# Optimization experiments

Measured on AMD Instinct MI355X. Metric: run time of the kernel, lower is better.

Reference implementation:

```python
import jax, jax.numpy as jnp
import numpy as np

B, N, C, H = 64, 197, 768, 12
CH = C // H            # 64 head dim
RC = CH // 2           # 32 reduced channel
RN = N // 8            # 24 reduced tokens
TOPK_COEF = 8
BUDGET = int(np.ceil(0.25 * N))   # 50
BASIS_THRESH = 0.02
MP_SCALE = H ** -0.5               # MaskPredictor: num_heads**-0.5 (as in source)
ATTN_SCALE = CH ** -0.5
LN_EPS = 1e-5


def _ln(x, g, b):
    mu = x.mean(-1, keepdims=True)
    var = ((x - mu) ** 2).mean(-1, keepdims=True)
    return (x - mu) * jax.lax.rsqrt(var + LN_EPS) * g + b


def _keep_topk(x, k):
    # zero all but the k largest along last axis (tie-break by value threshold)
    kth = jax.lax.top_k(x, k)[0][..., -1:]
    return jnp.where(x >= kth, x, 0.0)


def setup_inputs() -> dict:
    key = jax.random.key(0)
    ks = jax.random.split(key, 20)
    d = {}
    d['x'] = jax.random.normal(ks[0], (B, N, C), jnp.float32)
    s = 0.02
    d['Wqkv'] = jax.random.normal(ks[1], (C, 3 * C), jnp.float32) * s
    d['Wcq'] = jax.random.normal(ks[2], (CH, RC), jnp.float32) * s
    d['bcq'] = jnp.zeros((RC,), jnp.float32)
    d['Wck'] = jax.random.normal(ks[3], (CH, RC), jnp.float32) * s
    d['bck'] = jnp.zeros((RC,), jnp.float32)
    d['proj_n'] = jax.random.normal(ks[4], (N, RN), jnp.float32) * s
    d['proj_back_n'] = jax.random.normal(ks[5], (N, RN), jnp.float32) * s
    d['Wproj'] = jax.random.normal(ks[6], (C, C), jnp.float32) * s
    d['bproj'] = jnp.zeros((C,), jnp.float32)
    d['g1'] = jnp.ones((C,), jnp.float32)
    d['b1'] = jnp.zeros((C,), jnp.float32)
    d['g2'] = jnp.ones((C,), jnp.float32)
    d['b2'] = jnp.zeros((C,), jnp.float32)
    d['W1'] = jax.random.normal(ks[7], (C, 4 * C), jnp.float32) * s
    d['bfc1'] = jnp.zeros((4 * C,), jnp.float32)
    d['W2'] = jax.random.normal(ks[8], (4 * C, C), jnp.float32) * s
    d['bfc2'] = jnp.zeros((C,), jnp.float32)
    return d


def reference(x, Wqkv, Wcq, bcq, Wck, bck, proj_n, proj_back_n, Wproj, bproj,
              g1, b1, g2, b2, W1, bfc1, W2, bfc2):
    h = _ln(x, g1, b1)
    qkv = (h @ Wqkv).reshape(B, N, 3, H, CH).transpose(2, 0, 3, 1, 4)  # [3,B,H,N,CH]
    q, k, v = qkv[0], qkv[1], qkv[2]

    # ---- MaskPredictor (eval path) ----
    qp = q @ Wcq + bcq                                # [B,H,N,RC]
    kp = k @ Wck + bck                                # [B,H,N,RC]
    kk = jnp.einsum('bhnc,nr->bhcr', kp, proj_n)      # [B,H,RC,RN]
    cheap = jnp.einsum('bhnc,bhcr->bhnr', qp, kk) * MP_SCALE
    cheap = cheap[:, :, 1:, :]                        # drop cls query row
    basis_coef = jax.nn.softmax(cheap, axis=-1)       # [B,H,N-1,RN]
    basis_coef = _keep_topk(basis_coef, TOPK_COEF)
    basis = jnp.abs(proj_back_n.T)                    # [RN,N]
    basis = jnp.where(basis > BASIS_THRESH, basis, 0.0)
    approx_attn = basis_coef @ basis                  # [B,H,N-1,N]
    kth = jax.lax.top_k(approx_attn, BUDGET)[0][..., -1:]
    mask = approx_attn >= kth                         # [B,H,N-1,N] bool
    cls_mask = jnp.ones((B, H, 1, N), bool)
    attn_mask = jnp.concatenate([cls_mask, mask], axis=2)  # [B,H,N,N]

    # ---- masked full attention ----
    attn = jnp.einsum('bhqc,bhkc->bhqk', q * ATTN_SCALE, k)
    attn = jnp.where(attn_mask, attn, -jnp.inf)
    attn = jax.nn.softmax(attn, axis=-1)
    out = jnp.einsum('bhqk,bhkc->bhqc', attn, v)
    out = out.transpose(0, 2, 1, 3).reshape(B, N, C)
    out = out @ Wproj + bproj

    x = x + out                                       # skip_lam = 1.0
    h2 = _ln(x, g2, b2)
    mlp = jax.nn.gelu(h2 @ W1 + bfc1, approximate=False) @ W2 + bfc2
    x = x + mlp
    return x
```

## Files before the change

### kernel.cpp

```cpp
#include <hip/hip_runtime.h>
#include <math.h>
#include <float.h>

#define B_ 64
#define N_ 197
#define C_ 768
#define H_ 12
#define CH_ 64
#define RC_ 32
#define RN_ 24

typedef __attribute__((ext_vector_type(8))) short short8;
typedef __attribute__((ext_vector_type(4))) float f32x4;
typedef __attribute__((address_space(3))) void  lds_void;
typedef __attribute__((address_space(1))) const void g_void;

__device__ __forceinline__ float warp_sum(float v){
  #pragma unroll
  for(int o=32;o>=1;o>>=1) v += __shfl_xor(v,o);
  return v;
}
__device__ __forceinline__ float warp_max(float v){
  #pragma unroll
  for(int o=32;o>=1;o>>=1) v = fmaxf(v,__shfl_xor(v,o));
  return v;
}
__device__ __forceinline__ unsigned short f2bf(float f){
  union{float f; unsigned u;} c; c.f = f;
  unsigned r = c.u + 0x7FFF + ((c.u>>16)&1);
  return (unsigned short)(r>>16);
}
__device__ __forceinline__ float bf2f(unsigned short u){
  union{unsigned u; float f;} c; c.u = ((unsigned)u)<<16; return c.f;
}
__device__ __forceinline__ int2 xcd_swz(int gx, int gy){
  int nwg = gx*gy;
  int id = blockIdx.x + gx*blockIdx.y;
  int xcd = id & 7, loc = id >> 3;
  int q = nwg >> 3, r = nwg & 7;
  int swz = (xcd < r ? xcd*(q+1) : r*(q+1) + (xcd-r)*q) + loc;
  return make_int2(swz % gx, swz / gx);
}

__global__ __launch_bounds__(256) void ln_kernel(const float* __restrict__ x,
    const float* __restrict__ g, const float* __restrict__ bb, unsigned short* __restrict__ out){
  int r = blockIdx.x; int tid = threadIdx.x;
  const float* xr = x + (size_t)r*C_;
  float v0=xr[tid], v1=xr[tid+256], v2=xr[tid+512];
  __shared__ float red[8];
  float s = warp_sum(v0+v1+v2);
  if((tid&63)==0) red[tid>>6]=s;
  __syncthreads();
  float mu = (red[0]+red[1]+red[2]+red[3]) * (1.f/768.f);
  float d0=v0-mu,d1=v1-mu,d2=v2-mu;
  float s2 = warp_sum(d0*d0+d1*d1+d2*d2);
  if((tid&63)==0) red[4+(tid>>6)]=s2;
  __syncthreads();
  float rinv = rsqrtf((red[4]+red[5]+red[6]+red[7])*(1.f/768.f)+1e-5f);
  unsigned short* orow = out + (size_t)r*C_;
  orow[tid]     = f2bf(d0*rinv*g[tid]    +bb[tid]);
  orow[tid+256] = f2bf(d1*rinv*g[tid+256]+bb[tid+256]);
  orow[tid+512] = f2bf(d2*rinv*g[tid+512]+bb[tid+512]);
}

__global__ __launch_bounds__(256) void wtrans_kernel(const float* __restrict__ in,
    unsigned short* __restrict__ out, int K, int N){
  __shared__ float tile[32][33];
  int n0 = blockIdx.x*32, k0 = blockIdx.y*32;
  int tx = threadIdx.x&31, ty = threadIdx.x>>5;
  #pragma unroll
  for(int i=0;i<4;++i) tile[ty+8*i][tx] = in[(size_t)(k0+ty+8*i)*N + n0+tx];
  __syncthreads();
  #pragma unroll
  for(int i=0;i<4;++i) out[(size_t)(n0+ty+8*i)*K + k0+tx] = f2bf(tile[tx][ty+8*i]);
}

__global__ __launch_bounds__(256) void wcprep_kernel(const float* __restrict__ Wcq,
    const float* __restrict__ Wck, unsigned short* __restrict__ WcqT,
    unsigned short* __restrict__ WckT){
  int t = blockIdx.x*256 + threadIdx.x;
  if(t < 2048){
    int c = t>>6, k = t&63;
    WcqT[t] = f2bf(Wcq[k*32+c]);
    WckT[t] = f2bf(Wck[k*32+c]);
  }
}

template<int ACT, int RESID, int OUTBF16>
__global__ __launch_bounds__(256) void gemm_bf16(
    const unsigned short* __restrict__ A, const unsigned short* __restrict__ WT,
    const float* __restrict__ bias, const float* __restrict__ resid,
    void* __restrict__ Cout, int M, int K, int Nc){
  __shared__ unsigned short As[2*128*32];
  __shared__ unsigned short Bs[2*128*32];
  int tid = threadIdx.x, lane = tid&63, wid = tid>>6;
  int2 bxy = xcd_swz(gridDim.x, gridDim.y);
  int m0 = bxy.y*128, n0 = bxy.x*128;
  int wr = wid>>1, wc = wid&1;
  int lm = lane&15, lg = lane>>4;
  int row0 = tid>>2,         kc0 = (tid&3)*8;
  int row1 = (256+tid)>>2,   kc1 = (tid&3)*8;
  int ar0 = m0+row0; if(ar0 > M-1) ar0 = M-1;
  int ar1 = m0+row1; if(ar1 > M-1) ar1 = M-1;
  const unsigned short* gA0 = A  + (size_t)ar0*K + kc0;
  const unsigned short* gA1 = A  + (size_t)ar1*K + kc1;
  const unsigned short* gB0 = WT + (size_t)(n0+row0)*K + kc0;
  const unsigned short* gB1 = WT + (size_t)(n0+row1)*K + kc1;
  unsigned short* lA0 = As + (wid*64)*8;
  unsigned short* lA1 = As + (256 + wid*64)*8;
  unsigned short* lB0 = Bs + (wid*64)*8;
  unsigned short* lB1 = Bs + (256 + wid*64)*8;

#define STAGE_(buf, kt) do{ \
    __builtin_amdgcn_global_load_lds((g_void*)(gA0 + (kt)), (lds_void*)(lA0 + (buf)*4096), 16, 0, 0); \
    __builtin_amdgcn_global_load_lds((g_void*)(gB0 + (kt)), (lds_void*)(lB0 + (buf)*4096), 16, 0, 0); \
    __builtin_amdgcn_global_load_lds((g_void*)(gA1 + (kt)), (lds_void*)(lA1 + (buf)*4096), 16, 0, 0); \
    __builtin_amdgcn_global_load_lds((g_void*)(gB1 + (kt)), (lds_void*)(lB1 + (buf)*4096), 16, 0, 0); \
  }while(0)

  f32x4 acc[4][4] = {};
  const int nt = K/32;
  STAGE_(0, 0);
  __syncthreads();
  for(int t=0; t<nt; t+=2){
    STAGE_(1, (t+1)*32);
    {
      short8 af[4], bfv[4];
      #pragma unroll
      for(int i=0;i<4;++i){
        af[i]  = *(const short8*)(As + (64*wr + 16*i + lm)*32 + lg*8);
        bfv[i] = *(const short8*)(Bs + (64*wc + 16*i + lm)*32 + lg*8);
      }
      #pragma unroll
      for(int i=0;i<4;++i)
        #pragma unroll
        for(int j=0;j<4;++j)
          acc[i][j] = __builtin_amdgcn_mfma_f32_16x16x32_bf16(af[i], bfv[j], acc[i][j], 0,0,0);
    }
    __syncthreads();
    if(t+2 < nt) STAGE_(0, (t+2)*32);
    {
      short8 af[4], bfv[4];
      #pragma unroll
      for(int i=0;i<4;++i){
        af[i]  = *(const short8*)(As + 4096 + (64*wr + 16*i + lm)*32 + lg*8);
        bfv[i] = *(const short8*)(Bs + 4096 + (64*wc + 16*i + lm)*32 + lg*8);
      }
      #pragma unroll
      for(int i=0;i<4;++i)
        #pragma unroll
        for(int j=0;j<4;++j)
          acc[i][j] = __builtin_amdgcn_mfma_f32_16x16x32_bf16(af[i], bfv[j], acc[i][j], 0,0,0);
    }
    __syncthreads();
  }
#undef STAGE_
  #pragma unroll
  for(int i=0;i<4;++i){
    #pragma unroll
    for(int j=0;j<4;++j){
      int gcol = n0 + 64*wc + 16*j + lm;
      float bv = bias ? bias[gcol] : 0.f;
      #pragma unroll
      for(int r=0;r<4;++r){
        int grow = m0 + 64*wr + 16*i + lg*4 + r;
        if(grow < M){
          float cv = acc[i][j][r] + bv;
          if(ACT==1){
            float xx = cv;
            float p = xx*fmaf(xx*xx, 0.10294517f, 2.3022079f);
            float q = exp2f(p);
            cv = xx - xx*__builtin_amdgcn_rcpf(1.0f+q);
          }
          if(RESID) cv += resid[(size_t)grow*Nc + gcol];
          if(OUTBF16) ((unsigned short*)Cout)[(size_t)grow*Nc+gcol] = f2bf(cv);
          else        ((float*)Cout)[(size_t)grow*Nc+gcol] = cv;
        }
      }
    }
  }
}

template<int ACT, int RESID, int OUTBF16>
__global__ __launch_bounds__(512, 4) void gemm256_bf16(
    const unsigned short* __restrict__ A, const unsigned short* __restrict__ WT,
    const float* __restrict__ bias, const float* __restrict__ resid,
    void* __restrict__ Cout, int M, int K, int Nc){
  __shared__ unsigned short As[2*256*32];
  __shared__ unsigned short Bs[2*128*32];
  int tid = threadIdx.x, lane = tid&63, wid = tid>>6;
  int2 bxy = xcd_swz(gridDim.x, gridDim.y);
  int m0 = bxy.y*256, n0 = bxy.x*128;
  int wm = wid>>1, wn = wid&1;
  int lm = lane&15, lg = lane>>4;
  int rowA0 = tid>>2, rowA1 = 128 + (tid>>2), rowB = tid>>2;
  int kc = (tid&3)*8;
  int arA0 = m0+rowA0; if(arA0 > M-1) arA0 = M-1;
  int arA1 = m0+rowA1; if(arA1 > M-1) arA1 = M-1;
  const unsigned short* gA0 = A  + (size_t)arA0*K + kc;
  const unsigned short* gA1 = A  + (size_t)arA1*K + kc;
  const unsigned short* gB0 = WT + (size_t)(n0+rowB)*K + kc;
  unsigned short* lA0 = As + wid*512;
  unsigned short* lA1 = As + 4096 + wid*512;
  unsigned short* lB0 = Bs + wid*512;

#define STAGE2_(buf, kt) do{ \
    __builtin_amdgcn_global_load_lds((g_void*)(gA0 + (kt)), (lds_void*)(lA0 + (buf)*8192), 16, 0, 0); \
    __builtin_amdgcn_global_load_lds((g_void*)(gB0 + (kt)), (lds_void*)(lB0 + (buf)*4096), 16, 0, 0); \
    __builtin_amdgcn_global_load_lds((g_void*)(gA1 + (kt)), (lds_void*)(lA1 + (buf)*8192), 16, 0, 0); \
  }while(0)

  f32x4 acc[4][4] = {};
  const int nt = K/32;
  STAGE2_(0, 0);
  __syncthreads();
  for(int t=0; t<nt; ++t){
    int buf = t&1;
    if(t+1 < nt) STAGE2_(buf^1, (t+1)*32);
    const unsigned short* abase = As + buf*8192;
    const unsigned short* bbase = Bs + buf*4096;
    short8 af[4], bfv[4];
    #pragma unroll
    for(int i=0;i<4;++i)
      af[i] = *(const short8*)(abase + (wm*64 + i*16 + lm)*32 + lg*8);
    #pragma unroll
    for(int j=0;j<4;++j)
      bfv[j] = *(const short8*)(bbase + (wn*64 + j*16 + lm)*32 + lg*8);
    __builtin_amdgcn_s_setprio(1);
    #pragma unroll
    for(int i=0;i<4;++i)
      #pragma unroll
      for(int j=0;j<4;++j)
        acc[i][j] = __builtin_amdgcn_mfma_f32_16x16x32_bf16(af[i], bfv[j], acc[i][j], 0,0,0);
    __builtin_amdgcn_s_setprio(0);
    __syncthreads();
  }
#undef STAGE2_
  #pragma unroll
  for(int i=0;i<4;++i){
    #pragma unroll
    for(int j=0;j<4;++j){
      int gcol = n0 + wn*64 + j*16 + lm;
      float bv = bias ? bias[gcol] : 0.f;
      #pragma unroll
      for(int r=0;r<4;++r){
        int grow = m0 + wm*64 + i*16 + lg*4 + r;
        if(grow < M){
          float cv = acc[i][j][r] + bv;
          if(ACT==1){
            float xx = cv;
            float p = xx*fmaf(xx*xx, 0.10294517f, 2.3022079f);
            float q = exp2f(p);
            cv = xx - xx*__builtin_amdgcn_rcpf(1.0f+q);
          }
          if(RESID) cv += resid[(size_t)grow*Nc + gcol];
          if(OUTBF16) ((unsigned short*)Cout)[(size_t)grow*Nc+gcol] = f2bf(cv);
          else        ((float*)Cout)[(size_t)grow*Nc+gcol] = cv;
        }
      }
    }
  }
}

__global__ __launch_bounds__(512) void cheap_kernel(
    const unsigned short* __restrict__ qkv,
    const unsigned short* __restrict__ WcqT, const float* __restrict__ bcq,
    const unsigned short* __restrict__ WckT, const float* __restrict__ bck,
    const float* __restrict__ proj_n, float* __restrict__ coef){
  int bh = blockIdx.x; int b = bh/H_, h = bh%H_;
  int tid = threadIdx.x, lane = tid&63, wv = tid>>6;
  int lm = lane&15, lg = lane>>4;
  __shared__ __align__(16) unsigned short KQ[208*64];
  __shared__ __align__(16) float P2T[32*212];
  __shared__ __align__(16) float PNT[24*200];
  __shared__ float KK[768];
  const unsigned short* Kbase = qkv + ((size_t)(b*N_)*3 + 1)*C_ + h*CH_;
  const unsigned short* Qbase = qkv + ((size_t)(b*N_)*3 + 0)*C_ + h*CH_;
  for(int idx = tid; idx < 208*32; idx += 512){
    int k = idx>>5, cp = idx&31;
    unsigned v = (k < N_) ? *(const unsigned*)(Kbase + (size_t)k*3*C_ + cp*2) : 0u;
    unsigned off = (unsigned)(k*128 + cp*4) ^ ((unsigned)(k&7)<<4);
    *(unsigned*)((char*)KQ + off) = v;
  }
  for(int idx = tid; idx < 24*200; idx += 512){
    int r = idx/200, n = idx - r*200;
    PNT[idx] = (n < N_) ? proj_n[n*24+r] : 0.f;
  }
  __syncthreads();
  {
    short8 bfr[2][2];
    #pragma unroll
    for(int j=0;j<2;++j)
      #pragma unroll
      for(int s=0;s<2;++s)
        bfr[j][s] = *(const short8*)(WckT + (j*16+lm)*64 + s*32 + lg*8);
    float bias[2] = { bck[lm], bck[16+lm] };
    for(int t=wv; t<13; t+=8){
      int row = t*16 + lm;
      unsigned o0 = (unsigned)(row*128 + lg*16) ^ ((unsigned)(row&7)<<4);
      unsigned o1 = (unsigned)(row*128 + 64 + lg*16) ^ ((unsigned)(row&7)<<4);
      short8 a0 = *(const short8*)((char*)KQ + o0);
      short8 a1 = *(const short8*)((char*)KQ + o1);
      #pragma unroll
      for(int j=0;j<2;++j){
        f32x4 acc = (f32x4){0.f,0.f,0.f,0.f};
        acc = __builtin_amdgcn_mfma_f32_16x16x32_bf16(a0, bfr[j][0], acc, 0,0,0);
        acc = __builtin_amdgcn_mfma_f32_16x16x32_bf16(a1, bfr[j][1], acc, 0,0,0);
        #pragma unroll
        for(int r=0;r<4;++r)
          P2T[(j*16+lm)*212 + t*16 + lg*4 + r] = acc[r] + bias[j];
      }
    }
  }
  __syncthreads();
  {
    int i0 = tid, i1 = tid + 512;
    bool has1 = (i1 < 768);
    int c0 = i0/24, r0 = i0 - c0*24;
    int c1 = has1 ? i1/24 : 0, r1 = has1 ? (i1 - (i1/24)*24) : 0;
    float a0=0.f, a1=0.f;
    for(int n=0;n<200;n+=4){
      float4 x0 = *(const float4*)&P2T[c0*212+n];
      float4 p0 = *(const float4*)&PNT[r0*200+n];
      a0 += x0.x*p0.x; a0 += x0.y*p0.y; a0 += x0.z*p0.z; a0 += x0.w*p0.w;
      if(has1){
        float4 x1 = *(const float4*)&P2T[c1*212+n];
        float4 p1 = *(const float4*)&PNT[r1*200+n];
        a1 += x1.x*p1.x; a1 += x1.y*p1.y; a1 += x1.z*p1.z; a1 += x1.w*p1.w;
      }
    }
    KK[i0] = a0;
    if(has1) KK[i1] = a1;
    for(int idx = tid; idx < 197*32; idx += 512){
      int k = idx>>5, cp = idx&31;
      unsigned v = *(const unsigned*)(Qbase + (size_t)k*3*C_ + cp*2);
      unsigned off = (unsigned)(k*128 + cp*4) ^ ((unsigned)(k&7)<<4);
      *(unsigned*)((char*)KQ + off) = v;
    }
  }
  __syncthreads();
  float* QP = P2T;
  {
    short8 bfr[2][2];
    #pragma unroll
    for(int j=0;j<2;++j)
      #pragma unroll
      for(int s=0;s<2;++s)
        bfr[j][s] = *(const short8*)(WcqT + (j*16+lm)*64 + s*32 + lg*8);
    float bias[2] = { bcq[lm], bcq[16+lm] };
    for(int t=wv; t<13; t+=8){
      int row = t*16 + lm;
      unsigned o0 = (unsigned)(row*128 + lg*16) ^ ((unsigned)(row&7)<<4);
      unsigned o1 = (unsigned)(row*128 + 64 + lg*16) ^ ((unsigned)(row&7)<<4);
      short8 a0 = *(const short8*)((char*)KQ + o0);
      short8 a1 = *(const short8*)((char*)KQ + o1);
      #pragma unroll
      for(int j=0;j<2;++j){
        f32x4 acc = (f32x4){0.f,0.f,0.f,0.f};
        acc = __builtin_amdgcn_mfma_f32_16x16x32_bf16(a0, bfr[j][0], acc, 0,0,0);
        acc = __builtin_amdgcn_mfma_f32_16x16x32_bf16(a1, bfr[j][1], acc, 0,0,0);
        #pragma unroll
        for(int r=0;r<4;++r)
          QP[(t*16 + lg*4 + r)*32 + j*16 + lm] = acc[r] + bias[j];
      }
    }
  }
  __syncthreads();
  int l32 = lane & 31, half = lane >> 5;
  bool act = l32 < RN_;
  int ll = act ? l32 : 0;
  float kkreg[32];
  #pragma unroll
  for(int c=0;c<32;++c) kkreg[c] = KK[c*24 + ll];
  for(int i2 = wv*2; i2 < 196; i2 += 16){
    int i = i2 + half;
    int n = i + 1;
    float accv = 0.f;
    #pragma unroll
    for(int q=0;q<8;++q){
      float4 v4 = *(const float4*)&QP[n*32 + q*4];
      accv += v4.x*kkreg[q*4];   accv += v4.y*kkreg[q*4+1];
      accv += v4.z*kkreg[q*4+2]; accv += v4.w*kkreg[q*4+3];
    }
    float val = act ? accv * 0.28867513459481287f : -INFINITY;
    float m = val;
    #pragma unroll
    for(int o=16;o>=1;o>>=1) m = fmaxf(m, __shfl_xor(m, o));
    float e = act ? expf(val - m) : 0.f;
    float ssum = e;
    #pragma unroll
    for(int o=16;o>=1;o>>=1) ssum += __shfl_xor(ssum, o);
    float p = e/ssum;
    unsigned u = __float_as_uint(e);
    unsigned pL=0, pH=0;
    #pragma unroll
    for(int bit=30; bit>=0; --bit){
      unsigned tL = pL | (1u<<bit), tH = pH | (1u<<bit);
      unsigned thr = half ? tH : tL;
      unsigned long long bal = __ballot(u >= thr);
      int cL = __popcll(bal & 0xFFFFFFull);
      int cH = __popcll((bal>>32) & 0xFFFFFFull);
      if(cL>=8) pL=tL;
      if(cH>=8) pH=tH;
    }
    unsigned myp = half ? pH : pL;
    if(act) coef[((size_t)bh*196 + i)*24 + l32] = (u >= myp) ? p : 0.f;
  }
}

__global__ __launch_bounds__(256) void basis_kernel(const float* __restrict__ pb,
    float* __restrict__ basis){
  int t = blockIdx.x*256 + threadIdx.x;
  if(t < RN_*N_){
    int r = t/N_, j = t%N_;
    float v = fabsf(pb[(size_t)j*RN_ + r]);
    basis[t] = (v > 0.02f) ? v : 0.f;
  }
}

__global__ __launch_bounds__(256) void mask5_kernel(const float* __restrict__ coef,
    const float* __restrict__ basis, unsigned int* __restrict__ maskw){
  __shared__ float Bs[24*256];
  int tid = threadIdx.x, lane = tid&63, wv = tid>>6;
  for(int idx = tid; idx < 24*256; idx += 256){
    int r = idx>>8, q = idx&255;
    int e = ((q&3)<<6) | (q>>2);
    Bs[idx] = (e < N_) ? basis[r*N_ + e] : 0.f;
  }
  __syncthreads();
  int rowbase = blockIdx.x*16 + wv*4;
  float4 av[4];
  unsigned done = 0;
  #pragma unroll
  for(int j=0;j<4;++j){
    int row = rowbase + j;
    int qi = row % N_; int bh = row / N_;
    if(qi==0){
      if(lane<8){
        unsigned v = (lane<6)?0xFFFFFFFFu:((lane==6)?0x1Fu:0u);
        maskw[(size_t)row*8+lane]=v;
      }
      av[j] = make_float4(0.f,0.f,0.f,0.f);
      done |= (1u<<j);
    } else {
      float cfv = (lane<24) ? coef[((size_t)bh*196 + (qi-1))*24 + lane] : 0.f;
      unsigned long long nz = __ballot(cfv != 0.f);
      float4 a = make_float4(0.f,0.f,0.f,0.f);
      while(nz){
        int r = __ffsll((unsigned long long)nz) - 1;
        nz &= nz - 1;
        float c = __uint_as_float(__builtin_amdgcn_readlane(__float_as_uint(cfv), r));
        float4 bv = *(const float4*)&Bs[r*256 + lane*4];
        a.x += c*bv.x; a.y += c*bv.y; a.z += c*bv.z; a.w += c*bv.w;
      }
      av[j] = a;
    }
  }
  unsigned u[4][4];
  #pragma unroll
  for(int j=0;j<4;++j){
    u[j][0]=__float_as_uint(av[j].x); u[j][1]=__float_as_uint(av[j].y);
    u[j][2]=__float_as_uint(av[j].z); u[j][3]=__float_as_uint(av[j].w);
  }
  unsigned prefix[4] = {0,0,0,0};
  for(int bit=30; bit>=0; --bit){
    if(done == 0xFu) break;
    #pragma unroll
    for(int j=0;j<4;++j){
      unsigned t = prefix[j] | (1u<<bit);
      int c = __popcll(__ballot(u[j][0] >= t)) + __popcll(__ballot(u[j][1] >= t))
            + __popcll(__ballot(u[j][2] >= t)) + __popcll(__ballot(u[j][3] >= t));
      bool actj = !((done>>j)&1u);
      if(actj && c >= 50) prefix[j] = t;
      if(actj && c == 50) done |= (1u<<j);
    }
  }
  #pragma unroll
  for(int j=0;j<4;++j){
    int row = rowbase + j;
    if(row % N_ == 0) continue;
    #pragma unroll
    for(int r=0;r<4;++r){
      bool valid = (r<3) | (lane<5);
      bool keep = valid && (u[j][r] >= prefix[j]);
      unsigned long long bal = __ballot(keep);
      if(lane==0){
        maskw[(size_t)row*8 + 2*r]   = (unsigned)(bal & 0xFFFFFFFFull);
        maskw[(size_t)row*8 + 2*r+1] = (unsigned)(bal>>32);
      }
    }
  }
}

__global__ __launch_bounds__(512) void attn3_kernel(const unsigned short* __restrict__ qkv,
    const unsigned int* __restrict__ maskw, unsigned short* __restrict__ attn_out){
  int bh = blockIdx.x; int b = bh/H_, h = bh%H_;
  int tid = threadIdx.x, lane = tid&63, wv = tid>>6;
  int g = lane>>4, c16 = lane&15;
  __shared__ unsigned short Kb[208*64];
  __shared__ unsigned short Vt[64*220];
  __shared__ unsigned short Pl[8*16*224];
  __shared__ unsigned int   Ml[8][16][8];
  const unsigned short* Kbase = qkv + ((size_t)(b*N_)*3 + 1)*C_ + h*CH_;
  const unsigned short* Vbase = qkv + ((size_t)(b*N_)*3 + 2)*C_ + h*CH_;
  for(int idx = tid; idx < 208*32; idx += 512){
    int k = idx>>5, cp = idx&31;
    unsigned pk = 0;
    if(k < N_) pk = *(const unsigned*)(Kbase + (size_t)k*3*C_ + cp*2);
    unsigned off = (unsigned)(k*128 + cp*4) ^ ((unsigned)(k&7)<<4);
    *(unsigned*)((char*)Kb + off) = pk;
  }
  for(int idx = tid; idx < 64*110; idx += 512){
    int kp = idx>>6, c = idx&63;
    int k0 = kp*2, k1 = kp*2+1;
    unsigned v0 = (k0<N_) ? Vbase[(size_t)k0*3*C_ + c] : 0;
    unsigned v1 = (k1<N_) ? Vbase[(size_t)k1*3*C_ + c] : 0;
    *(unsigned*)((char*)Vt + c*440 + kp*4) = v0 | (v1<<16);
  }
  __syncthreads();
  size_t pbase = (size_t)wv*16*448;
  for(int i=lane;i<128;i+=64){
    int ql = i>>3; int kk = 208 + (i&7)*2;
    unsigned off = (unsigned)(ql*448 + kk*2) ^ ((unsigned)(ql&7)<<4);
    *(unsigned*)((char*)Pl + pbase + off) = 0u;
  }
  for(int t = wv; t < 13; t += 8){
    int qb = t*16;
    for(int i = lane; i < 128; i += 64){
      int row = i>>3, word = i&7;
      int qr = qb+row; if(qr>196) qr=196;
      Ml[wv][row][word] = maskw[(size_t)(bh*N_+qr)*8 + word];
    }
    int qrow = qb + c16; if(qrow>196) qrow=196;
    const unsigned short* Qr = qkv + ((size_t)(b*N_+qrow)*3)*C_ + h*CH_ + g*8;
    short8 af[2];
    af[0] = *(const short8*)(Qr);
    af[1] = *(const short8*)(Qr + 32);
    f32x4 sf[13];
    #pragma unroll
    for(int f=0;f<13;++f){
      sf[f] = (f32x4){0.f,0.f,0.f,0.f};
      #pragma unroll
      for(int s=0;s<2;++s){
        int row = f*16 + c16;
        unsigned off = (unsigned)(row*128 + s*64 + g*16) ^ ((unsigned)(row&7)<<4);
        short8 bfr = *(const short8*)((char*)Kb + off);
        sf[f] = __builtin_amdgcn_mfma_f32_16x16x32_bf16(af[s], bfr, sf[f], 0,0,0);
      }
      sf[f][0]*=0.125f; sf[f][1]*=0.125f; sf[f][2]*=0.125f; sf[f][3]*=0.125f;
    }
    unsigned keep[4] = {0,0,0,0};
    float m[4] = {-FLT_MAX,-FLT_MAX,-FLT_MAX,-FLT_MAX};
    #pragma unroll
    for(int f=0;f<13;++f)
      #pragma unroll
      for(int r=0;r<4;++r){
        unsigned bit = (Ml[wv][g*4+r][f>>1] >> ((f&1)*16 + c16)) & 1u;
        keep[r] |= bit<<f;
        if(bit) m[r] = fmaxf(m[r], sf[f][r]);
      }
    #pragma unroll
    for(int r=0;r<4;++r){
      #pragma unroll
      for(int o=8;o>=1;o>>=1) m[r] = fmaxf(m[r], __shfl_xor(m[r], o));
    }
    float sum[4] = {0,0,0,0};
    #pragma unroll
    for(int f=0;f<13;++f)
      #pragma unroll
      for(int r=0;r<4;++r){
        float e = ((keep[r]>>f)&1u) ? expf(sf[f][r]-m[r]) : 0.f;
        sf[f][r] = e; sum[r] += e;
      }
    #pragma unroll
    for(int r=0;r<4;++r){
      #pragma unroll
      for(int o=8;o>=1;o>>=1) sum[r] += __shfl_xor(sum[r], o);
      sum[r] = 1.f/sum[r];
    }
    #pragma unroll
    for(int f=0;f<13;++f)
      #pragma unroll
      for(int r=0;r<4;++r){
        int ql = g*4+r;
        unsigned off = (unsigned)(ql*448 + (f*16+c16)*2) ^ ((unsigned)(ql&7)<<4);
        *(unsigned short*)((char*)Pl + pbase + off) = f2bf(sf[f][r]*sum[r]);
      }
    #pragma unroll
    for(int ct=0;ct<4;++ct){
      f32x4 oa = (f32x4){0.f,0.f,0.f,0.f};
      #pragma unroll
      for(int ks=0;ks<7;++ks){
        unsigned offa = (unsigned)(c16*448 + (ks*32+g*8)*2) ^ ((unsigned)(c16&7)<<4);
        short8 pa = *(const short8*)((char*)Pl + pbase + offa);
        short8 vb = *(const short8*)((char*)Vt + (size_t)(ct*16+c16)*440 + (ks*32+g*8)*2);
        oa = __builtin_amdgcn_mfma_f32_16x16x32_bf16(pa, vb, oa, 0,0,0);
      }
      #pragma unroll
      for(int r=0;r<4;++r){
        int qq = qb + g*4 + r;
        if(qq < N_)
          attn_out[((size_t)(b*N_+qq))*C_ + h*CH_ + ct*16 + c16] = f2bf(oa[r]);
      }
    }
  }
}

extern "C" void kernel_launch(void* const* d_in, const int* in_sizes, int n_in,
                              void* d_out, int out_size, void* d_ws, size_t ws_size,
                              hipStream_t stream){
  const float* x    =(const float*)d_in[0];
  const float* Wqkv =(const float*)d_in[1];
  const float* Wcq  =(const float*)d_in[2];
  const float* bcq  =(const float*)d_in[3];
  const float* Wck  =(const float*)d_in[4];
  const float* bck  =(const float*)d_in[5];
  const float* proj_n=(const float*)d_in[6];
  const float* proj_back_n=(const float*)d_in[7];
  const float* Wproj=(const float*)d_in[8];
  const float* bproj=(const float*)d_in[9];
  const float* g1=(const float*)d_in[10];
  const float* b1=(const float*)d_in[11];
  const float* g2=(const float*)d_in[12];
  const float* b2=(const float*)d_in[13];
  const float* W1=(const float*)d_in[14];
  const float* bfc1=(const float*)d_in[15];
  const float* W2=(const float*)d_in[16];
  const float* bfc2=(const float*)d_in[17];
  float* out=(float*)d_out;

  float* ws=(float*)d_ws;
  size_t off=0;
  unsigned short* hbuf = (unsigned short*)(ws+off); off += (size_t)12608*768/2;
  size_t qkv_off = off;
  unsigned short* qkv = (unsigned short*)(ws+off); off += (size_t)12608*2304/2;
  off += (size_t)768*197*32;
  off += (size_t)768*197*32;
  off += (size_t)768*32*24;
  float* coef = ws+off;        off += (size_t)768*196*24;
  float* basis= ws+off;        off += 4736;
  unsigned int* maskw=(unsigned int*)(ws+off); off += (size_t)768*197*8;
  unsigned short* WqkvT = (unsigned short*)(ws+off); off += (size_t)2304*768/2;
  unsigned short* WprojT= (unsigned short*)(ws+off); off += (size_t)768*768/2;
  unsigned short* W1T   = (unsigned short*)(ws+off); off += (size_t)3072*768/2;
  unsigned short* W2T   = (unsigned short*)(ws+off); off += (size_t)768*3072/2;
  unsigned short* WcqT  = (unsigned short*)(ws+off); off += 1024;
  unsigned short* WckT  = (unsigned short*)(ws+off); off += 1024;
  unsigned short* attn_out = hbuf;
  unsigned short* hidden = (unsigned short*)(ws+qkv_off);
  float* x1 = out;

  wtrans_kernel<<<dim3(72,24),256,0,stream>>>(Wqkv, WqkvT, 768, 2304);
  wtrans_kernel<<<dim3(24,24),256,0,stream>>>(Wproj, WprojT, 768, 768);
  wtrans_kernel<<<dim3(96,24),256,0,stream>>>(W1, W1T, 768, 3072);
  wtrans_kernel<<<dim3(24,96),256,0,stream>>>(W2, W2T, 3072, 768);
  wcprep_kernel<<<8,256,0,stream>>>(Wcq, Wck, WcqT, WckT);
  ln_kernel<<<12608,256,0,stream>>>(x,g1,b1,hbuf);
  gemm256_bf16<0,0,1><<<dim3(18,50),512,0,stream>>>(hbuf,WqkvT,nullptr,nullptr,qkv,12608,768,2304);
  cheap_kernel<<<768,512,0,stream>>>(qkv,WcqT,bcq,WckT,bck,proj_n,coef);
  basis_kernel<<<19,256,0,stream>>>(proj_back_n,basis);
  mask5_kernel<<<9456,256,0,stream>>>(coef,basis,maskw);
  attn3_kernel<<<768,512,0,stream>>>(qkv,maskw,attn_out);
  gemm_bf16<0,1,0><<<dim3(6,99),256,0,stream>>>(attn_out,WprojT,bproj,x,x1,12608,768,768);
  ln_kernel<<<12608,256,0,stream>>>(x1,g2,b2,hbuf);
  gemm256_bf16<1,0,1><<<dim3(24,50),512,0,stream>>>(hbuf,W1T,bfc1,nullptr,hidden,12608,768,3072);
  gemm_bf16<0,1,0><<<dim3(6,99),256,0,stream>>>(hidden,W2T,bfc2,x1,out,12608,3072,768);
}
```

Baseline: 655.3 us.

## Deepen K-tile to 64 with XOR-swizzled LDS in gemm_bf16; unroll mask coef loop

The 128x128 bf16 GEMM used for the projection and FC2 now stages a K-tile of 64 instead of 32. LDS columns are XOR-swizzled to avoid bank conflicts, and MFMA issue is wrapped in s_setprio with launch bounds set for two blocks per CU. This halves the number of barriers per K and increases work per stage, at the cost of doubling LDS usage. Separately, the mask kernel's variable-length sparse accumulation loop becomes a fixed 8-slot unrolled gather, so LDS loads can be issued together, at the cost of wasted slots when fewer than 8 coefficients are nonzero.

```diff
diff --git a/kernel.cpp b/kernel.cpp
--- a/kernel.cpp
+++ b/kernel.cpp
@@ -87,70 +87,64 @@
 }
 
 template<int ACT, int RESID, int OUTBF16>
-__global__ __launch_bounds__(256) void gemm_bf16(
+__global__ __launch_bounds__(256, 2) void gemm_bf16(
     const unsigned short* __restrict__ A, const unsigned short* __restrict__ WT,
     const float* __restrict__ bias, const float* __restrict__ resid,
     void* __restrict__ Cout, int M, int K, int Nc){
-  __shared__ unsigned short As[2*128*32];
-  __shared__ unsigned short Bs[2*128*32];
+  __shared__ unsigned short As[2*128*64];
+  __shared__ unsigned short Bs[2*128*64];
   int tid = threadIdx.x, lane = tid&63, wid = tid>>6;
   int2 bxy = xcd_swz(gridDim.x, gridDim.y);
   int m0 = bxy.y*128, n0 = bxy.x*128;
   int wr = wid>>1, wc = wid&1;
   int lm = lane&15, lg = lane>>4;
-  int row0 = tid>>2,         kc0 = (tid&3)*8;
-  int row1 = (256+tid)>>2,   kc1 = (tid&3)*8;
-  int ar0 = m0+row0; if(ar0 > M-1) ar0 = M-1;
-  int ar1 = m0+row1; if(ar1 > M-1) ar1 = M-1;
-  const unsigned short* gA0 = A  + (size_t)ar0*K + kc0;
-  const unsigned short* gA1 = A  + (size_t)ar1*K + kc1;
-  const unsigned short* gB0 = WT + (size_t)(n0+row0)*K + kc0;
-  const unsigned short* gB1 = WT + (size_t)(n0+row1)*K + kc1;
-  unsigned short* lA0 = As + (wid*64)*8;
-  unsigned short* lA1 = As + (256 + wid*64)*8;
-  unsigned short* lB0 = Bs + (wid*64)*8;
-  unsigned short* lB1 = Bs + (256 + wid*64)*8;
+  const unsigned short *gA[4], *gB[4];
+  #pragma unroll
+  for(int i=0;i<4;++i){
+    int cid = tid + 256*i;
+    int srow = cid>>3;
+    int sc = (cid&7) ^ (srow&7);
+    int ar = m0 + srow; if(ar > M-1) ar = M-1;
+    gA[i] = A  + (size_t)ar*K + sc*8;
+    gB[i] = WT + (size_t)(n0+srow)*K + sc*8;
+  }
+  unsigned short* lAb = As + wid*512;
+  unsigned short* lBb = Bs + wid*512;
 
 #define STAGE_(buf, kt) do{ \
-    __builtin_amdgcn_global_load_lds((g_void*)(gA0 + (kt)), (lds_void*)(lA0 + (buf)*4096), 16, 0, 0); \
-    __builtin_amdgcn_global_load_lds((g_void*)(gB0 + (kt)), (lds_void*)(lB0 + (buf)*4096), 16, 0, 0); \
-    __builtin_amdgcn_global_load_lds((g_void*)(gA1 + (kt)), (lds_void*)(lA1 + (buf)*4096), 16, 0, 0); \
-    __builtin_amdgcn_global_load_lds((g_void*)(gB1 + (kt)), (lds_void*)(lB1 + (buf)*4096), 16, 0, 0); \
+    _Pragma("unroll") \
+    for(int i=0;i<4;++i){ \
+      __builtin_amdgcn_global_load_lds((g_void*)(gA[i] + (kt)), (lds_void*)(lAb + (buf)*8192 + i*2048), 16, 0, 0); \
+      __builtin_amdgcn_global_load_lds((g_void*)(gB[i] + (kt)), (lds_void*)(lBb + (buf)*8192 + i*2048), 16, 0, 0); \
+    } \
   }while(0)
 
   f32x4 acc[4][4] = {};
-  const int nt = K/32;
+  const int nt = K/64;
   STAGE_(0, 0);
   __syncthreads();
-  for(int t=0; t<nt; t+=2){
-    STAGE_(1, (t+1)*32);
-    {
+  for(int t=0; t<nt; ++t){
+    int buf = t&1;
+    if(t+1 < nt) STAGE_(buf^1, (t+1)*64);
+    const unsigned short* abase = As + buf*8192;
+    const unsigned short* bbase = Bs + buf*8192;
+    #pragma unroll
+    for(int s=0; s<2; ++s){
+      int ch = ((s*4+lg) ^ (lm&7)) * 8;
       short8 af[4], bfv[4];
       #pragma unroll
-      for(int i=0;i<4;++i){
-        af[i]  = *(const short8*)(As + (64*wr + 16*i + lm)*32 + lg*8);
-        bfv[i] = *(const short8*)(Bs + (64*wc + 16*i + lm)*32 + lg*8);
-      }
+      for(int i=0;i<4;++i)
+        af[i]  = *(const short8*)(abase + (64*wr + 16*i + lm)*64 + ch);
+      #pragma unroll
+      for(int j=0;j<4;++j)
+        bfv[j] = *(const short8*)(bbase + (64*wc + 16*j + lm)*64 + ch);
+      __builtin_amdgcn_s_setprio(1);
       #pragma unroll
       for(int i=0;i<4;++i)
         #pragma unroll
         for(int j=0;j<4;++j)
           acc[i][j] = __builtin_amdgcn_mfma_f32_16x16x32_bf16(af[i], bfv[j], acc[i][j], 0,0,0);
-    }
-    __syncthreads();
-    if(t+2 < nt) STAGE_(0, (t+2)*32);
-    {
-      short8 af[4], bfv[4];
-      #pragma unroll
-      for(int i=0;i<4;++i){
-        af[i]  = *(const short8*)(As + 4096 + (64*wr + 16*i + lm)*32 + lg*8);
-        bfv[i] = *(const short8*)(Bs + 4096 + (64*wc + 16*i + lm)*32 + lg*8);
-      }
-      #pragma unroll
-      for(int i=0;i<4;++i)
-        #pragma unroll
-        for(int j=0;j<4;++j)
-          acc[i][j] = __builtin_amdgcn_mfma_f32_16x16x32_bf16(af[i], bfv[j], acc[i][j], 0,0,0);
+      __builtin_amdgcn_s_setprio(0);
     }
     __syncthreads();
   }
@@ -418,7 +412,7 @@
   }
 }
 
-__global__ __launch_bounds__(256) void mask5_kernel(const float* __restrict__ coef,
+__global__ __launch_bounds__(256) void mask6_kernel(const float* __restrict__ coef,
     const float* __restrict__ basis, unsigned int* __restrict__ maskw){
   __shared__ float Bs[24*256];
   int tid = threadIdx.x, lane = tid&63, wv = tid>>6;
@@ -445,13 +439,25 @@
     } else {
       float cfv = (lane<24) ? coef[((size_t)bh*196 + (qi-1))*24 + lane] : 0.f;
       unsigned long long nz = __ballot(cfv != 0.f);
+      int rr[8];
+      #pragma unroll
+      for(int s=0;s<8;++s){
+        rr[s] = nz ? (__ffsll(nz)-1) : 64;
+        nz &= nz - 1;
+      }
+      float cc[8]; float4 bv[8];
+      #pragma unroll
+      for(int s=0;s<8;++s){
+        int r = (rr[s] < 64) ? rr[s] : 0;
+        float c = __uint_as_float(__builtin_amdgcn_readlane(__float_as_uint(cfv), r));
+        cc[s] = (rr[s] < 64) ? c : 0.f;
+        bv[s] = *(const float4*)&Bs[r*256 + lane*4];
+      }
       float4 a = make_float4(0.f,0.f,0.f,0.f);
-      while(nz){
-        int r = __ffsll((unsigned long long)nz) - 1;
-        nz &= nz - 1;
-        float c = __uint_as_float(__builtin_amdgcn_readlane(__float_as_uint(cfv), r));
-        float4 bv = *(const float4*)&Bs[r*256 + lane*4];
-        a.x += c*bv.x; a.y += c*bv.y; a.z += c*bv.z; a.w += c*bv.w;
+      #pragma unroll
+      for(int s=0;s<8;++s){
+        a.x += cc[s]*bv[s].x; a.y += cc[s]*bv[s].y;
+        a.z += cc[s]*bv[s].z; a.w += cc[s]*bv[s].w;
       }
       av[j] = a;
     }
@@ -659,7 +665,7 @@
   gemm256_bf16<0,0,1><<<dim3(18,50),512,0,stream>>>(hbuf,WqkvT,nullptr,nullptr,qkv,12608,768,2304);
   cheap_kernel<<<768,512,0,stream>>>(qkv,WcqT,bcq,WckT,bck,proj_n,coef);
   basis_kernel<<<19,256,0,stream>>>(proj_back_n,basis);
-  mask5_kernel<<<9456,256,0,stream>>>(coef,basis,maskw);
+  mask6_kernel<<<9456,256,0,stream>>>(coef,basis,maskw);
   attn3_kernel<<<768,512,0,stream>>>(qkv,maskw,attn_out);
   gemm_bf16<0,1,0><<<dim3(6,99),256,0,stream>>>(attn_out,WprojT,bproj,x,x1,12608,768,768);
   ln_kernel<<<12608,256,0,stream>>>(x1,g2,b2,hbuf);
```

Result: slower. 711.8 us (+8.6%).

## Fuse mask construction into cheap attention kernel, eliminating coef round-trip

Applied to the files above, without the earlier changes.

The approximate-attention top-k mask computation (basis matmul plus the 50-budget radix select) is folded into cheap_kernel, so each wave computes its two coef rows and immediately builds their mask words from a basis table staged in reused LDS. This removes the mask5 kernel launch and the global write and read of the coef tensor. The top-8 radix select also gains early exit once exactly 8 values are found. The cost is longer per-wave work in cheap_kernel, only 768 blocks of parallelism for the mask stage, and extra register pressure from the unrolled 8-term gather.

```diff
diff --git a/kernel.cpp b/kernel.cpp
--- a/kernel.cpp
+++ b/kernel.cpp
@@ -266,7 +266,8 @@
     const unsigned short* __restrict__ qkv,
     const unsigned short* __restrict__ WcqT, const float* __restrict__ bcq,
     const unsigned short* __restrict__ WckT, const float* __restrict__ bck,
-    const float* __restrict__ proj_n, float* __restrict__ coef){
+    const float* __restrict__ proj_n, const float* __restrict__ basis,
+    unsigned int* __restrict__ maskw){
   int bh = blockIdx.x; int b = bh/H_, h = bh%H_;
   int tid = threadIdx.x, lane = tid&63, wv = tid>>6;
   int lm = lane&15, lg = lane>>4;
@@ -366,6 +367,17 @@
     }
   }
   __syncthreads();
+  float* Bs2 = (float*)KQ;
+  for(int idx = tid; idx < 24*256; idx += 512){
+    int r = idx>>8, q = idx&255;
+    int e = ((q&3)<<6) | (q>>2);
+    Bs2[idx] = (e < N_) ? basis[r*N_ + e] : 0.f;
+  }
+  if(tid < 8){
+    unsigned v = (tid<6)?0xFFFFFFFFu:((tid==6)?0x1Fu:0u);
+    maskw[(size_t)(bh*N_)*8 + tid] = v;
+  }
+  __syncthreads();
   int l32 = lane & 31, half = lane >> 5;
   bool act = l32 < RN_;
   int ll = act ? l32 : 0;
@@ -392,19 +404,79 @@
     for(int o=16;o>=1;o>>=1) ssum += __shfl_xor(ssum, o);
     float p = e/ssum;
     unsigned u = __float_as_uint(e);
-    unsigned pL=0, pH=0;
-    #pragma unroll
+    unsigned pL=0, pH=0; bool dL=false, dH=false;
     for(int bit=30; bit>=0; --bit){
+      if(dL && dH) break;
       unsigned tL = pL | (1u<<bit), tH = pH | (1u<<bit);
       unsigned thr = half ? tH : tL;
       unsigned long long bal = __ballot(u >= thr);
       int cL = __popcll(bal & 0xFFFFFFull);
       int cH = __popcll((bal>>32) & 0xFFFFFFull);
-      if(cL>=8) pL=tL;
-      if(cH>=8) pH=tH;
+      if(!dL && cL>=8){ pL=tL; if(cL==8) dL=true; }
+      if(!dH && cH>=8){ pH=tH; if(cH==8) dH=true; }
     }
     unsigned myp = half ? pH : pL;
-    if(act) coef[((size_t)bh*196 + i)*24 + l32] = (u >= myp) ? p : 0.f;
+    float cf = (act && u >= myp) ? p : 0.f;
+    unsigned long long nzall = __ballot(cf != 0.f);
+    float4 aAB[2];
+    #pragma unroll
+    for(int rw=0; rw<2; ++rw){
+      unsigned nz = (unsigned)((nzall >> (rw*32)) & 0xFFFFFFull);
+      int base = rw*32;
+      int rr[8];
+      #pragma unroll
+      for(int s=0;s<8;++s){ rr[s] = nz ? (__ffs(nz)-1) : 64; nz &= nz ? (nz-1) : 0; }
+      float cc[8]; float4 bv[8];
+      #pragma unroll
+      for(int s=0;s<8;++s){
+        int r = (rr[s] < 64) ? rr[s] : 0;
+        float c = __uint_as_float(__builtin_amdgcn_readlane(__float_as_uint(cf), base + r));
+        cc[s] = (rr[s] < 64) ? c : 0.f;
+        bv[s] = *(const float4*)&Bs2[r*256 + lane*4];
+      }
+      float4 a = make_float4(0.f,0.f,0.f,0.f);
+      #pragma unroll
+      for(int s=0;s<8;++s){
+        a.x += cc[s]*bv[s].x; a.y += cc[s]*bv[s].y;
+        a.z += cc[s]*bv[s].z; a.w += cc[s]*bv[s].w;
+      }
+      while(nz){
+        int r = __ffs(nz)-1; nz &= nz-1;
+        float c = __uint_as_float(__builtin_amdgcn_readlane(__float_as_uint(cf), base + r));
+        float4 b4 = *(const float4*)&Bs2[r*256 + lane*4];
+        a.x += c*b4.x; a.y += c*b4.y; a.z += c*b4.z; a.w += c*b4.w;
+      }
+      aAB[rw] = a;
+    }
+    unsigned uA[4] = {__float_as_uint(aAB[0].x),__float_as_uint(aAB[0].y),
+                      __float_as_uint(aAB[0].z),__float_as_uint(aAB[0].w)};
+    unsigned uB[4] = {__float_as_uint(aAB[1].x),__float_as_uint(aAB[1].y),
+                      __float_as_uint(aAB[1].z),__float_as_uint(aAB[1].w)};
+    unsigned qA=0, qB=0; bool dA=false, dB=false;
+    for(int bit=30; bit>=0; --bit){
+      if(dA && dB) break;
+      unsigned tA = qA | (1u<<bit), tB = qB | (1u<<bit);
+      int cA = __popcll(__ballot(uA[0] >= tA)) + __popcll(__ballot(uA[1] >= tA))
+             + __popcll(__ballot(uA[2] >= tA)) + __popcll(__ballot(uA[3] >= tA));
+      int cB = __popcll(__ballot(uB[0] >= tB)) + __popcll(__ballot(uB[1] >= tB))
+             + __popcll(__ballot(uB[2] >= tB)) + __popcll(__ballot(uB[3] >= tB));
+      if(!dA && cA>=50){ qA=tA; if(cA==50) dA=true; }
+      if(!dB && cB>=50){ qB=tB; if(cB==50) dB=true; }
+    }
+    size_t rowA = (size_t)bh*N_ + (i2+1);
+    size_t rowB = (size_t)bh*N_ + (i2+2);
+    #pragma unroll
+    for(int r=0;r<4;++r){
+      bool valid = (r<3) | (lane<5);
+      unsigned long long balA = __ballot(valid && (uA[r] >= qA));
+      unsigned long long balB = __ballot(valid && (uB[r] >= qB));
+      if(lane==0){
+        maskw[rowA*8 + 2*r]   = (unsigned)(balA & 0xFFFFFFFFull);
+        maskw[rowA*8 + 2*r+1] = (unsigned)(balA>>32);
+        maskw[rowB*8 + 2*r]   = (unsigned)(balB & 0xFFFFFFFFull);
+        maskw[rowB*8 + 2*r+1] = (unsigned)(balB>>32);
+      }
+    }
   }
 }
 
@@ -415,80 +487,6 @@
     int r = t/N_, j = t%N_;
     float v = fabsf(pb[(size_t)j*RN_ + r]);
     basis[t] = (v > 0.02f) ? v : 0.f;
-  }
-}
-
-__global__ __launch_bounds__(256) void mask5_kernel(const float* __restrict__ coef,
-    const float* __restrict__ basis, unsigned int* __restrict__ maskw){
-  __shared__ float Bs[24*256];
-  int tid = threadIdx.x, lane = tid&63, wv = tid>>6;
-  for(int idx = tid; idx < 24*256; idx += 256){
-    int r = idx>>8, q = idx&255;
-    int e = ((q&3)<<6) | (q>>2);
-    Bs[idx] = (e < N_) ? basis[r*N_ + e] : 0.f;
-  }
-  __syncthreads();
-  int rowbase = blockIdx.x*16 + wv*4;
-  float4 av[4];
-  unsigned done = 0;
-  #pragma unroll
-  for(int j=0;j<4;++j){
-    int row = rowbase + j;
-    int qi = row % N_; int bh = row / N_;
-    if(qi==0){
-      if(lane<8){
-        unsigned v = (lane<6)?0xFFFFFFFFu:((lane==6)?0x1Fu:0u);
-        maskw[(size_t)row*8+lane]=v;
-      }
-      av[j] = make_float4(0.f,0.f,0.f,0.f);
-      done |= (1u<<j);
-    } else {
-      float cfv = (lane<24) ? coef[((size_t)bh*196 + (qi-1))*24 + lane] : 0.f;
-      unsigned long long nz = __ballot(cfv != 0.f);
-      float4 a = make_float4(0.f,0.f,0.f,0.f);
-      while(nz){
-        int r = __ffsll((unsigned long long)nz) - 1;
-        nz &= nz - 1;
-        float c = __uint_as_float(__builtin_amdgcn_readlane(__float_as_uint(cfv), r));
-        float4 bv = *(const float4*)&Bs[r*256 + lane*4];
-        a.x += c*bv.x; a.y += c*bv.y; a.z += c*bv.z; a.w += c*bv.w;
-      }
-      av[j] = a;
-    }
-  }
-  unsigned u[4][4];
-  #pragma unroll
-  for(int j=0;j<4;++j){
-    u[j][0]=__float_as_uint(av[j].x); u[j][1]=__float_as_uint(av[j].y);
-    u[j][2]=__float_as_uint(av[j].z); u[j][3]=__float_as_uint(av[j].w);
-  }
-  unsigned prefix[4] = {0,0,0,0};
-  for(int bit=30; bit>=0; --bit){
-    if(done == 0xFu) break;
-    #pragma unroll
-    for(int j=0;j<4;++j){
-      unsigned t = prefix[j] | (1u<<bit);
-      int c = __popcll(__ballot(u[j][0] >= t)) + __popcll(__ballot(u[j][1] >= t))
-            + __popcll(__ballot(u[j][2] >= t)) + __popcll(__ballot(u[j][3] >= t));
-      bool actj = !((done>>j)&1u);
-      if(actj && c >= 50) prefix[j] = t;
-      if(actj && c == 50) done |= (1u<<j);
-    }
-  }
-  #pragma unroll
-  for(int j=0;j<4;++j){
-    int row = rowbase + j;
-    if(row % N_ == 0) continue;
-    #pragma unroll
-    for(int r=0;r<4;++r){
-      bool valid = (r<3) | (lane<5);
-      bool keep = valid && (u[j][r] >= prefix[j]);
-      unsigned long long bal = __ballot(keep);
-      if(lane==0){
-        maskw[(size_t)row*8 + 2*r]   = (unsigned)(bal & 0xFFFFFFFFull);
-        maskw[(size_t)row*8 + 2*r+1] = (unsigned)(bal>>32);
-      }
-    }
   }
 }
 
@@ -637,7 +635,7 @@
   off += (size_t)768*197*32;
   off += (size_t)768*197*32;
   off += (size_t)768*32*24;
-  float* coef = ws+off;        off += (size_t)768*196*24;
+  off += (size_t)768*196*24;
   float* basis= ws+off;        off += 4736;
   unsigned int* maskw=(unsigned int*)(ws+off); off += (size_t)768*197*8;
   unsigned short* WqkvT = (unsigned short*)(ws+off); off += (size_t)2304*768/2;
@@ -657,9 +655,8 @@
   wcprep_kernel<<<8,256,0,stream>>>(Wcq, Wck, WcqT, WckT);
   ln_kernel<<<12608,256,0,stream>>>(x,g1,b1,hbuf);
   gemm256_bf16<0,0,1><<<dim3(18,50),512,0,stream>>>(hbuf,WqkvT,nullptr,nullptr,qkv,12608,768,2304);
-  cheap_kernel<<<768,512,0,stream>>>(qkv,WcqT,bcq,WckT,bck,proj_n,coef);
   basis_kernel<<<19,256,0,stream>>>(proj_back_n,basis);
-  mask5_kernel<<<9456,256,0,stream>>>(coef,basis,maskw);
+  cheap_kernel<<<768,512,0,stream>>>(qkv,WcqT,bcq,WckT,bck,proj_n,basis,maskw);
   attn3_kernel<<<768,512,0,stream>>>(qkv,maskw,attn_out);
   gemm_bf16<0,1,0><<<dim3(6,99),256,0,stream>>>(attn_out,WprojT,bproj,x,x1,12608,768,768);
   ln_kernel<<<12608,256,0,stream>>>(x1,g2,b2,hbuf);
```

Result: slower. 691.1 us (+5.5%).
